# Optimization experiments

Hardware: AMD Instinct MI355X
Metric: run time of the kernel (lower is better)

The kernel has to match this reference:

```python
import jax, jax.numpy as jnp
import numpy as np

N_NODES = 50000
N_EDGES = 20000
NNZ = 500000


def _degrees(node_idx, edge_idx):
    ones = jnp.ones((node_idx.shape[0],), dtype=jnp.float32)
    deg_e = jax.ops.segment_sum(ones, edge_idx, num_segments=N_EDGES)
    deg_v = jax.ops.segment_sum(ones, node_idx, num_segments=N_NODES)
    return jnp.maximum(deg_e, 1.0)[:, None], jnp.maximum(deg_v, 1.0)[:, None]


def hgnn_conv(X, W, b, node_idx, edge_idx, deg_e, deg_v):
    # X: [V, Fin] -> project, V->E mean scatter, E->V mean gather (HGNN conv)
    H = X @ W                                                     # [V, Fout]
    e_feat = jax.ops.segment_sum(H[node_idx], edge_idx, num_segments=N_EDGES) / deg_e  # [E, Fout]
    v_feat = jax.ops.segment_sum(e_feat[edge_idx], node_idx, num_segments=N_NODES) / deg_v  # [V, Fout]
    return v_feat + b


def setup_inputs() -> dict:
    key = jax.random.key(0)
    ks = jax.random.split(key, 6)
    X = jax.random.normal(ks[0], (N_NODES, 256), dtype=jnp.float32)
    node_idx = jax.random.randint(ks[1], (NNZ,), 0, N_NODES, dtype=jnp.int32)
    edge_idx = jax.random.randint(ks[2], (NNZ,), 0, N_EDGES, dtype=jnp.int32)
    W1 = jax.random.normal(ks[3], (256, 256), dtype=jnp.float32) / np.sqrt(256.0)
    W2 = jax.random.normal(ks[4], (256, 256), dtype=jnp.float32) / np.sqrt(256.0)
    W3 = jax.random.normal(ks[5], (256, 40), dtype=jnp.float32) / np.sqrt(256.0)
    return {"X": X, "node_idx": node_idx, "edge_idx": edge_idx,
            "W1": W1, "b1": jnp.zeros((256,), jnp.float32),
            "W2": W2, "b2": jnp.zeros((256,), jnp.float32),
            "W3": W3, "b3": jnp.zeros((40,), jnp.float32)}


def reference(X, node_idx, edge_idx, W1, b1, W2, b2, W3, b3):
    deg_e, deg_v = _degrees(node_idx, edge_idx)
    # dropout layers are identity in eval mode
    H = jax.nn.relu(hgnn_conv(X, W1, b1, node_idx, edge_idx, deg_e, deg_v))
    H = jax.nn.relu(hgnn_conv(H, W2, b2, node_idx, edge_idx, deg_e, deg_v))
    H = hgnn_conv(H, W3, b3, node_idx, edge_idx, deg_e, deg_v)
    return jax.nn.log_softmax(H, axis=1)
```

## Files before the change

### kernel.cpp

```cpp
#include <hip/hip_runtime.h>
#include <math.h>

#define N_NODES 50000
#define N_EDGES 20000
#define NNZ_CT  500000
#define KDIM    256
#define K32     8

#define NB_RANK 62
#define CHUNK   8192
#define EW      5000
#define VW      12500

typedef __attribute__((ext_vector_type(8))) short    short8v;
typedef __attribute__((ext_vector_type(4))) float    f32x4;
typedef __attribute__((ext_vector_type(8))) unsigned short ushort8v;
typedef __attribute__((ext_vector_type(4))) unsigned short ushort4v;

#define GLD16(g, l) __builtin_amdgcn_global_load_lds( \
    (const __attribute__((address_space(1))) unsigned int*)(g), \
    (__attribute__((address_space(3))) unsigned int*)(l), 16, 0, 0)

__device__ __forceinline__ unsigned short bf16_rne(float f) {
    unsigned u = __float_as_uint(f);
    return (unsigned short)((u + 0x7FFFu + ((u >> 16) & 1u)) >> 16);
}
__device__ __forceinline__ float bf16_to_f(unsigned short h) {
    return __uint_as_float(((unsigned)h) << 16);
}
__device__ __forceinline__ void bf16_split(float f, unsigned short& h, unsigned short& l) {
    unsigned u = __float_as_uint(f);
    unsigned hb = (u + 0x7FFFu + ((u >> 16) & 1u)) >> 16;
    h = (unsigned short)hb;
    float r = f - __uint_as_float(hb << 16);
    unsigned ru = __float_as_uint(r);
    l = (unsigned short)((ru + 0x7FFFu + ((ru >> 16) & 1u)) >> 16);
}

__global__ __launch_bounds__(256) void rank_lds(
    const int* __restrict__ node_idx, const int* __restrict__ edge_idx,
    unsigned* __restrict__ bhe, unsigned* __restrict__ bhv,
    unsigned char* __restrict__ lrank_e, unsigned char* __restrict__ lrank_v)
{
    __shared__ unsigned hist[VW];
    int b = blockIdx.x;
    int i0 = b * CHUNK;
    int i1 = i0 + CHUNK; if (i1 > NNZ_CT) i1 = NNZ_CT;
    for (int w = threadIdx.x; w < EW; w += 256) hist[w] = 0;
    __syncthreads();
    for (int i = i0 + threadIdx.x; i < i1; i += 256) {
        int e = edge_idx[i];
        unsigned sh = 8u * (e & 3);
        unsigned old = atomicAdd(&hist[e >> 2], 1u << sh);
        lrank_e[i] = (unsigned char)((old >> sh) & 0xFFu);
    }
    __syncthreads();
    for (int w = threadIdx.x; w < EW; w += 256) bhe[b * EW + w] = hist[w];
    __syncthreads();
    for (int w = threadIdx.x; w < VW; w += 256) hist[w] = 0;
    __syncthreads();
    for (int i = i0 + threadIdx.x; i < i1; i += 256) {
        int v = node_idx[i];
        unsigned sh = 8u * (v & 3);
        unsigned old = atomicAdd(&hist[v >> 2], 1u << sh);
        lrank_v[i] = (unsigned char)((old >> sh) & 0xFFu);
    }
    __syncthreads();
    for (int w = threadIdx.x; w < VW; w += 256) bhv[b * VW + w] = hist[w];
}

__device__ __forceinline__ void conv_B_body(
    const float* __restrict__ B, unsigned short* __restrict__ Bh,
    unsigned short* __restrict__ Bl, int Ncols, int n16_count, int t)
{
    if (t >= n16_count * 512) return;
    int lane = t & 63, k32 = (t >> 6) & 7, n16 = t >> 9;
    int col = n16 * 16 + (lane & 15);
    int k0  = k32 * 32 + (lane >> 4) * 8;
    ushort8v h, l;
#pragma unroll
    for (int j = 0; j < 8; j++) {
        float f = (col < Ncols) ? B[(size_t)(k0 + j) * Ncols + col] : 0.f;
        unsigned short hh, ll; bf16_split(f, hh, ll); h[j] = hh; l[j] = ll;
    }
    size_t off = (((size_t)n16 * 8 + k32) << 9) + lane * 8;
    *(ushort8v*)(Bh + off) = h;
    *(ushort8v*)(Bl + off) = l;
}

__global__ __launch_bounds__(256) void mid_fuse(
    const unsigned* __restrict__ bhe, const unsigned* __restrict__ bhv,
    unsigned* __restrict__ bbase_e, unsigned* __restrict__ bbase_v,
    int* __restrict__ cnt_e, int* __restrict__ cnt_v,
    const float* __restrict__ X, unsigned short* __restrict__ Xb,
    const float* __restrict__ W1, unsigned short* __restrict__ W1h, unsigned short* __restrict__ W1l,
    const float* __restrict__ W2, unsigned short* __restrict__ W2h, unsigned short* __restrict__ W2l,
    const float* __restrict__ W3, unsigned short* __restrict__ W3h, unsigned short* __restrict__ W3l)
{
    int b0 = blockIdx.x;
    if (b0 < 69) {
        int t = b0 * 256 + threadIdx.x;
        if (t >= EW + VW) return;
        const unsigned* bh; unsigned* bb; int* cnt; int w;
        if (t < EW) { bh = bhe; bb = bbase_e; cnt = cnt_e; w = t; }
        else        { bh = bhv; bb = bbase_v; cnt = cnt_v; w = t - EW; }
        int stride = (t < EW) ? EW : VW;
        unsigned s0 = 0, s1 = 0, s2 = 0, s3 = 0;
#pragma unroll 2
        for (int b = 0; b < NB_RANK; ++b) {
            unsigned h = bh[(size_t)b * stride + w];
            bb[(size_t)b * stride + w] = s0 | (s1 << 8) | (s2 << 16) | (s3 << 24);
            s0 += h & 255u; s1 += (h >> 8) & 255u; s2 += (h >> 16) & 255u; s3 += (h >> 24);
        }
        *(int4*)(cnt + 4 * w) = make_int4((int)s0, (int)s1, (int)s2, (int)s3);
    } else if (b0 < 6319) {
        int t = (b0 - 69) * 256 + threadIdx.x;
        const float* src = X + (size_t)t * 8;
        float f[8];
        *(float4*)(f)     = *(const float4*)(src);
        *(float4*)(f + 4) = *(const float4*)(src + 4);
        ushort8v h;
#pragma unroll
        for (int j = 0; j < 8; j++) h[j] = bf16_rne(f[j]);
        *(ushort8v*)(Xb + (size_t)t * 8) = h;
    } else {
        int j = b0 - 6319;
        if (j < 32)      conv_B_body(W1, W1h, W1l, 256, 16, j * 256 + (int)threadIdx.x);
        else if (j < 64) conv_B_body(W2, W2h, W2l, 256, 16, (j - 32) * 256 + (int)threadIdx.x);
        else             conv_B_body(W3, W3h, W3l, 40,  8,  (j - 64) * 256 + (int)threadIdx.x);
    }
}

__global__ __launch_bounds__(1024) void scan_dual(
    const int* __restrict__ cnt_e, int* __restrict__ off_e, float* __restrict__ inv_e,
    const int* __restrict__ cnt_v, int* __restrict__ off_v, float* __restrict__ inv_v)
{
    const int* cnt; int* off; float* inv; int n;
    if (blockIdx.x == 0) { cnt = cnt_e; off = off_e; inv = inv_e; n = N_EDGES; }
    else                 { cnt = cnt_v; off = off_v; inv = inv_v; n = N_NODES; }
    __shared__ int wsum[16];
    __shared__ int carry_s;
    int tid = threadIdx.x, lane = tid & 63, wid = tid >> 6;
    if (tid == 0) carry_s = 0;
    __syncthreads();
    for (int base = 0; base < n; base += 4096) {
        int i4 = base + tid * 4;
        int4 x = make_int4(0, 0, 0, 0);
        if (i4 + 3 < n) x = *(const int4*)(cnt + i4);
        else if (i4 < n) {
            x.x = cnt[i4];
            if (i4 + 1 < n) x.y = cnt[i4 + 1];
            if (i4 + 2 < n) x.z = cnt[i4 + 2];
        }
        int s0 = x.x, s1 = s0 + x.y, s2 = s1 + x.z, s3 = s2 + x.w;
        int incl = s3;
#pragma unroll
        for (int o = 1; o < 64; o <<= 1) { int t = __shfl_up(incl, o, 64); if (lane >= o) incl += t; }
        if (lane == 63) wsum[wid] = incl;
        __syncthreads();
        if (wid == 0) {
            int v = (lane < 16) ? wsum[lane] : 0;
#pragma unroll
            for (int o = 1; o < 16; o <<= 1) { int t = __shfl_up(v, o, 64); if (lane >= o) v += t; }
            if (lane < 16) wsum[lane] = v;
        }
        __syncthreads();
        int wpre = (wid == 0) ? 0 : wsum[wid - 1];
        int carry = carry_s;
        int excl = carry + wpre + incl - s3;
        if (i4 < n) {
            int e0 = excl, e1 = excl + s0, e2 = excl + s1, e3 = excl + s2;
            if (i4 + 3 < n) { *(int4*)(off + i4) = make_int4(e0, e1, e2, e3); }
            else {
                off[i4] = e0;
                if (i4 + 1 < n) off[i4 + 1] = e1;
                if (i4 + 2 < n) off[i4 + 2] = e2;
            }
            inv[i4] = 1.0f / fmaxf((float)x.x, 1.0f);
            if (i4 + 1 < n) inv[i4 + 1] = 1.0f / fmaxf((float)x.y, 1.0f);
            if (i4 + 2 < n) inv[i4 + 2] = 1.0f / fmaxf((float)x.z, 1.0f);
            if (i4 + 3 < n) inv[i4 + 3] = 1.0f / fmaxf((float)x.w, 1.0f);
        }
        __syncthreads();
        if (tid == 1023) carry_s = carry + wpre + incl;
        __syncthreads();
    }
    if (tid == 0) off[n] = carry_s;
}

__global__ __launch_bounds__(256) void fill_part(
    const int* __restrict__ node_idx, const int* __restrict__ edge_idx,
    const unsigned char* __restrict__ lrank_e, const unsigned char* __restrict__ lrank_v,
    const unsigned* __restrict__ bbase_e, const unsigned* __restrict__ bbase_v,
    const int* __restrict__ off_e, const int* __restrict__ off_v,
    int* __restrict__ csr_e_nodes, int* __restrict__ csr_v_edges)
{
    int part = blockIdx.x & 7, blk = blockIdx.x >> 3, nblk = gridDim.x >> 3;
    int elo = part * (N_EDGES / 8), ehi = elo + N_EDGES / 8;
    int vlo = part * (N_NODES / 8), vhi = vlo + N_NODES / 8;
    for (int i = blk * 256 + threadIdx.x; i < NNZ_CT; i += nblk * 256) {
        int e = edge_idx[i], v = node_idx[i];
        int b = i >> 13;
        if (e >= elo && e < ehi) {
            unsigned bb = (bbase_e[(size_t)b * EW + (e >> 2)] >> (8u * (e & 3))) & 0xFFu;
            csr_e_nodes[off_e[e] + (int)bb + (int)lrank_e[i]] = v;
        }
        if (v >= vlo && v < vhi) {
            unsigned bb = (bbase_v[(size_t)b * VW + (v >> 2)] >> (8u * (v & 3))) & 0xFFu;
            csr_v_edges[off_v[v] + (int)bb + (int)lrank_v[i]] = e;
        }
    }
}

__global__ __launch_bounds__(256) void gemm_bf16(
    const unsigned short* __restrict__ At,
    const unsigned short* __restrict__ Bh, const unsigned short* __restrict__ Bl,
    unsigned short* __restrict__ C, int M, int Ncols, int ldC)
{
    __shared__ unsigned short lds[16384];
    const int tid  = threadIdx.x;
    const int lane = tid & 63, wid = tid >> 6;
    const int wr = wid >> 1, wc = wid & 1;
    const int m0t = blockIdx.y * 8;
    const int n0t = blockIdx.x * 8;

    f32x4 acc[4][4] = {};

    for (int k32 = 0; k32 < K32; ++k32) {
#pragma unroll
        for (int i = 0; i < 6; ++i) {
            int c = i * 4 + wid;
            if (c < 8) {
                const unsigned short* gA = At + (((size_t)(m0t + c) * 8 + k32) << 9) + lane * 8;
                GLD16(gA, &lds[c * 512 + lane * 8]);
            } else {
                int idx = c - 8, half = idx >> 3, st = idx & 7;
                const unsigned short* gB = (half ? Bl : Bh)
                    + (((size_t)(n0t + st) * 8 + k32) << 9) + lane * 8;
                GLD16(gB, &lds[4096 + idx * 512 + lane * 8]);
            }
        }
        __syncthreads();
        short8v a[4], bh[4], bl[4];
#pragma unroll
        for (int x = 0; x < 4; ++x) {
            a[x]  = *(const short8v*)&lds[(wr * 4 + x) * 512 + lane * 8];
            bh[x] = *(const short8v*)&lds[4096 + (wc * 4 + x) * 512 + lane * 8];
            bl[x] = *(const short8v*)&lds[4096 + (8 + wc * 4 + x) * 512 + lane * 8];
        }
#pragma unroll
        for (int mi = 0; mi < 4; ++mi)
#pragma unroll
            for (int ni = 0; ni < 4; ++ni) {
                acc[mi][ni] = __builtin_amdgcn_mfma_f32_16x16x32_bf16(a[mi], bh[ni], acc[mi][ni], 0, 0, 0);
                acc[mi][ni] = __builtin_amdgcn_mfma_f32_16x16x32_bf16(a[mi], bl[ni], acc[mi][ni], 0, 0, 0);
            }
        __syncthreads();
    }

    {
        const int rg = lane >> 4, cl = lane & 15;
        const int base = wid * 4096;
#pragma unroll
        for (int mi = 0; mi < 4; ++mi) {
            int swz = ((mi * 4 + rg) & 3) << 4;
#pragma unroll
            for (int ni = 0; ni < 4; ++ni) {
                int colf = (ni * 16 + cl) ^ swz;
#pragma unroll
                for (int r = 0; r < 4; ++r)
                    lds[base + (mi * 16 + rg * 4 + r) * 64 + colf] = bf16_rne(acc[mi][ni][r]);
            }
        }
    }
    __syncthreads();
    {
        int row = tid >> 1, half = tid & 1;
        int grow = blockIdx.y * 128 + row;
        if (grow < M) {
            int wsrc = (row >> 6) * 2 + half;
            int rl = row & 63;
            int swz = ((rl >> 2) & 3) << 4;
            unsigned short* dst = C + (size_t)grow * ldC + n0t * 16 + half * 64;
#pragma unroll
            for (int s = 0; s < 8; ++s) {
                int c0 = half * 64 + s * 8;
                if (n0t * 16 + c0 + 8 <= Ncols) {
                    ushort8v v = *(const ushort8v*)&lds[wsrc * 4096 + rl * 64 + ((s * 8) ^ swz)];
                    *(ushort8v*)(dst + s * 8) = v;
                }
            }
        }
    }
}

__global__ __launch_bounds__(256) void agg_e256_tiled(
    const unsigned short* __restrict__ src, unsigned short* __restrict__ Et,
    const int* __restrict__ offs, const int* __restrict__ lists,
    const float* __restrict__ invdeg)
{
    __shared__ unsigned short hbuf[16 * 264];
    int tid = threadIdx.x, lane = tid & 63, wid = tid >> 6;
    int e16 = blockIdx.x;
#pragma unroll
    for (int q = 0; q < 4; ++q) {
        int el = wid * 4 + q;
        int w = e16 * 16 + el;
        int s = offs[w], e = offs[w + 1];
        float a0 = 0.f, a1 = 0.f, a2 = 0.f, a3 = 0.f;
        for (int j = s; j < e; j += 8) {
            int r[8]; float m[8];
            r[0] = lists[j]; m[0] = 1.f;
#pragma unroll
            for (int u = 1; u < 8; ++u) {
                bool ok = (j + u) < e;
                r[u] = ok ? lists[j + u] : r[0];
                m[u] = ok ? 1.f : 0.f;
            }
            ushort4v v[8];
#pragma unroll
            for (int u = 0; u < 8; ++u)
                v[u] = *(const ushort4v*)(src + (size_t)r[u] * 256 + lane * 4);
            a0 += bf16_to_f(v[0][0]); a1 += bf16_to_f(v[0][1]);
            a2 += bf16_to_f(v[0][2]); a3 += bf16_to_f(v[0][3]);
#pragma unroll
            for (int u = 1; u < 8; ++u) {
                a0 = fmaf(m[u], bf16_to_f(v[u][0]), a0);
                a1 = fmaf(m[u], bf16_to_f(v[u][1]), a1);
                a2 = fmaf(m[u], bf16_to_f(v[u][2]), a2);
                a3 = fmaf(m[u], bf16_to_f(v[u][3]), a3);
            }
        }
        float sc = invdeg[w];
        ushort4v o;
        o[0] = bf16_rne(a0 * sc); o[1] = bf16_rne(a1 * sc);
        o[2] = bf16_rne(a2 * sc); o[3] = bf16_rne(a3 * sc);
        *(ushort4v*)&hbuf[el * 264 + lane * 4] = o;
    }
    __syncthreads();
#pragma unroll
    for (int u = 0; u < 2; ++u) {
        int sl = tid * 2 + u;
        int k32 = sl >> 6, lt = sl & 63;
        int row = lt & 15, hi = lt >> 4;
        int k0 = k32 * 32 + hi * 8;
        ushort8v v = *(const ushort8v*)&hbuf[row * 264 + k0];
        *(ushort8v*)(Et + (((size_t)e16 * 8 + k32) << 9) + lt * 8) = v;
    }
}

__global__ __launch_bounds__(256) void agg_v256_row(
    const unsigned short* __restrict__ src, unsigned short* __restrict__ Vb,
    const int* __restrict__ offs, const int* __restrict__ lists,
    const float* __restrict__ invdeg, const float* __restrict__ bias, int nseg)
{
    int w = (blockIdx.x * 256 + threadIdx.x) >> 6;
    int lane = threadIdx.x & 63;
    if (w >= nseg) return;
    int s = offs[w], e = offs[w + 1];
    float a0 = 0.f, a1 = 0.f, a2 = 0.f, a3 = 0.f;
    for (int j = s; j < e; j += 8) {
        int r[8]; float m[8];
        r[0] = lists[j]; m[0] = 1.f;
#pragma unroll
        for (int u = 1; u < 8; ++u) {
            bool ok = (j + u) < e;
            r[u] = ok ? lists[j + u] : r[0];
            m[u] = ok ? 1.f : 0.f;
        }
        ushort4v v[8];
#pragma unroll
        for (int u = 0; u < 8; ++u)
            v[u] = *(const ushort4v*)(src + (size_t)r[u] * 256 + lane * 4);
        a0 += bf16_to_f(v[0][0]); a1 += bf16_to_f(v[0][1]);
        a2 += bf16_to_f(v[0][2]); a3 += bf16_to_f(v[0][3]);
#pragma unroll
        for (int u = 1; u < 8; ++u) {
            a0 = fmaf(m[u], bf16_to_f(v[u][0]), a0);
            a1 = fmaf(m[u], bf16_to_f(v[u][1]), a1);
            a2 = fmaf(m[u], bf16_to_f(v[u][2]), a2);
            a3 = fmaf(m[u], bf16_to_f(v[u][3]), a3);
        }
    }
    float sc = invdeg[w];
    const float4 b = *(const float4*)(bias + lane * 4);
    ushort4v o;
    o[0] = bf16_rne(fmaxf(a0 * sc + b.x, 0.f));
    o[1] = bf16_rne(fmaxf(a1 * sc + b.y, 0.f));
    o[2] = bf16_rne(fmaxf(a2 * sc + b.z, 0.f));
    o[3] = bf16_rne(fmaxf(a3 * sc + b.w, 0.f));
    *(ushort4v*)(Vb + (size_t)w * 256 + lane * 4) = o;
}

__global__ __launch_bounds__(256) void agg_v256_blk(
    const unsigned short* __restrict__ src, unsigned short* __restrict__ At,
    const int* __restrict__ offs, const int* __restrict__ lists,
    const float* __restrict__ invdeg, const float* __restrict__ bias)
{
    __shared__ unsigned short hbuf[16 * 264];
    int tid = threadIdx.x, lane = tid & 63, wid = tid >> 6;
    int m16 = blockIdx.x;
    const float4 b = *(const float4*)(bias + lane * 4);
#pragma unroll
    for (int q = 0; q < 4; ++q) {
        int nl = wid * 4 + q;
        int w = m16 * 16 + nl;
        int s = offs[w], e = offs[w + 1];
        float a0 = 0.f, a1 = 0.f, a2 = 0.f, a3 = 0.f;
        for (int j = s; j < e; j += 8) {
            int r[8]; float m[8];
            r[0] = lists[j]; m[0] = 1.f;
#pragma unroll
            for (int u = 1; u < 8; ++u) {
                bool ok = (j + u) < e;
                r[u] = ok ? lists[j + u] : r[0];
                m[u] = ok ? 1.f : 0.f;
            }
            ushort4v v[8];
#pragma unroll
            for (int u = 0; u < 8; ++u)
                v[u] = *(const ushort4v*)(src + (size_t)r[u] * 256 + lane * 4);
            a0 += bf16_to_f(v[0][0]); a1 += bf16_to_f(v[0][1]);
            a2 += bf16_to_f(v[0][2]); a3 += bf16_to_f(v[0][3]);
#pragma unroll
            for (int u = 1; u < 8; ++u) {
                a0 = fmaf(m[u], bf16_to_f(v[u][0]), a0);
                a1 = fmaf(m[u], bf16_to_f(v[u][1]), a1);
                a2 = fmaf(m[u], bf16_to_f(v[u][2]), a2);
                a3 = fmaf(m[u], bf16_to_f(v[u][3]), a3);
            }
        }
        float sc = invdeg[w];
        ushort4v o;
        o[0] = bf16_rne(fmaxf(a0 * sc + b.x, 0.f));
        o[1] = bf16_rne(fmaxf(a1 * sc + b.y, 0.f));
        o[2] = bf16_rne(fmaxf(a2 * sc + b.z, 0.f));
        o[3] = bf16_rne(fmaxf(a3 * sc + b.w, 0.f));
        *(ushort4v*)&hbuf[nl * 264 + lane * 4] = o;
    }
    __syncthreads();
#pragma unroll
    for (int u = 0; u < 2; ++u) {
        int sl = tid * 2 + u;
        int k32 = sl >> 6, lt = sl & 63;
        int row = lt & 15, hi = lt >> 4;
        int k0 = k32 * 32 + hi * 8;
        ushort8v v = *(const ushort8v*)&hbuf[row * 264 + k0];
        *(ushort8v*)(At + (((size_t)m16 * 8 + k32) << 9) + lt * 8) = v;
    }
}

__global__ __launch_bounds__(256) void agg_mean40(
    const unsigned short* __restrict__ src, unsigned short* __restrict__ dst,
    const int* __restrict__ offs, const int* __restrict__ lists,
    const float* __restrict__ invdeg, int nseg)
{
    int w = (blockIdx.x * 256 + threadIdx.x) >> 6;
    int lane = threadIdx.x & 63;
    if (w >= nseg) return;
    int s = offs[w], e = offs[w + 1];
    if (lane < 40) {
        float acc = 0.f;
        for (int j = s; j < e; j += 8) {
            int r[8]; float m[8];
            r[0] = lists[j]; m[0] = 1.f;
#pragma unroll
            for (int u = 1; u < 8; ++u) {
                bool ok = (j + u) < e;
                r[u] = ok ? lists[j + u] : r[0];
                m[u] = ok ? 1.f : 0.f;
            }
            float v[8];
#pragma unroll
            for (int u = 0; u < 8; ++u)
                v[u] = bf16_to_f(src[(size_t)r[u] * 40 + lane]);
            acc += v[0];
#pragma unroll
            for (int u = 1; u < 8; ++u) acc = fmaf(m[u], v[u], acc);
        }
        dst[(size_t)w * 40 + lane] = bf16_rne(acc * invdeg[w]);
    }
}

__global__ __launch_bounds__(256) void agg_v40_lsm(
    const unsigned short* __restrict__ efeat, float* __restrict__ out,
    const int* __restrict__ offs, const int* __restrict__ lists,
    const float* __restrict__ invdeg, const float* __restrict__ bias,
    int nseg)
{
    int w = (blockIdx.x * 256 + threadIdx.x) >> 6;
    int lane = threadIdx.x & 63;
    if (w >= nseg) return;
    int s = offs[w], e = offs[w + 1];
    float acc = 0.f;
    if (lane < 40) {
        for (int j = s; j < e; j += 4) {
            int r[4]; float m[4];
            r[0] = lists[j]; m[0] = 1.f;
#pragma unroll
            for (int u = 1; u < 4; ++u) {
                bool ok = (j + u) < e;
                r[u] = ok ? lists[j + u] : r[0];
                m[u] = ok ? 1.f : 0.f;
            }
            float v[4];
#pragma unroll
            for (int u = 0; u < 4; ++u)
                v[u] = bf16_to_f(efeat[(size_t)r[u] * 40 + lane]);
            acc += v[0];
#pragma unroll
            for (int u = 1; u < 4; ++u) acc = fmaf(m[u], v[u], acc);
        }
    }
    float val = (lane < 40) ? (acc * invdeg[w] + bias[lane]) : -1e30f;
    float m = val;
#pragma unroll
    for (int o = 32; o; o >>= 1) m = fmaxf(m, __shfl_xor(m, o));
    float ex = (lane < 40) ? expf(val - m) : 0.f;
    float ssum = ex;
#pragma unroll
    for (int o = 32; o; o >>= 1) ssum += __shfl_xor(ssum, o);
    if (lane < 40) out[(size_t)w * 40 + lane] = val - m - logf(ssum);
}

extern "C" void kernel_launch(void* const* d_in, const int* in_sizes, int n_in,
                              void* d_out, int out_size, void* d_ws, size_t ws_size,
                              hipStream_t stream)
{
    const float* X        = (const float*)d_in[0];
    const int*   node_idx = (const int*)d_in[1];
    const int*   edge_idx = (const int*)d_in[2];
    const float* W1 = (const float*)d_in[3];
    const float* b1 = (const float*)d_in[4];
    const float* W2 = (const float*)d_in[5];
    const float* b2 = (const float*)d_in[6];
    const float* W3 = (const float*)d_in[7];
    const float* b3 = (const float*)d_in[8];
    float* out = (float*)d_out;

    char* p = (char*)d_ws;
    auto alloc = [&](size_t bytes) -> char* {
        char* r = p;
        p += (bytes + 255) & ~(size_t)255;
        return r;
    };
    int*   cnt_e = (int*)alloc((size_t)N_EDGES * 4);
    int*   cnt_v = (int*)alloc((size_t)N_NODES * 4);
    int*   off_e = (int*)alloc((size_t)(N_EDGES + 1) * 4);
    int*   off_v = (int*)alloc((size_t)(N_NODES + 1) * 4);
    float* inv_e = (float*)alloc((size_t)N_EDGES * 4);
    float* inv_v = (float*)alloc((size_t)N_NODES * 4);
    unsigned* bhe = (unsigned*)alloc((size_t)NB_RANK * EW * 4);
    unsigned* bhv = (unsigned*)alloc((size_t)NB_RANK * VW * 4);
    unsigned* bbase_e = (unsigned*)alloc((size_t)NB_RANK * EW * 4);
    unsigned* bbase_v = (unsigned*)alloc((size_t)NB_RANK * VW * 4);
    unsigned char* lrank_e = (unsigned char*)alloc((size_t)NNZ_CT);
    unsigned char* lrank_v = (unsigned char*)alloc((size_t)NNZ_CT);
    int*   csr_e = (int*)alloc((size_t)NNZ_CT * 4);
    int*   csr_v = (int*)alloc((size_t)NNZ_CT * 4);

    const int M16 = N_NODES / 16;
    const int M16_PAD = 391 * 8;
    const int E16 = N_EDGES / 16;
    const int E16_PAD = 157 * 8;
    unsigned short* Xb  = (unsigned short*)alloc((size_t)N_NODES * 256 * 2);
    unsigned short* At  = (unsigned short*)alloc((size_t)M16_PAD * 4096 * 2);
    unsigned short* Et  = (unsigned short*)alloc((size_t)E16_PAD * 4096 * 2);
    unsigned short* Ef  = (unsigned short*)alloc((size_t)N_EDGES * 256 * 2);
    unsigned short* W1h = (unsigned short*)alloc((size_t)16 * 4096 * 2);
    unsigned short* W1l = (unsigned short*)alloc((size_t)16 * 4096 * 2);
    unsigned short* W2h = (unsigned short*)alloc((size_t)16 * 4096 * 2);
    unsigned short* W2l = (unsigned short*)alloc((size_t)16 * 4096 * 2);
    unsigned short* W3h = (unsigned short*)alloc((size_t)8 * 4096 * 2);
    unsigned short* W3l = (unsigned short*)alloc((size_t)8 * 4096 * 2);
    unsigned short* C40 = (unsigned short*)alloc((size_t)N_NODES * 40 * 2);
    unsigned short* E40 = (unsigned short*)alloc((size_t)N_EDGES * 40 * 2);

    rank_lds<<<NB_RANK, 256, 0, stream>>>(node_idx, edge_idx, bhe, bhv, lrank_e, lrank_v);
    mid_fuse<<<6399, 256, 0, stream>>>(bhe, bhv, bbase_e, bbase_v, cnt_e, cnt_v,
                                       X, Xb, W1, W1h, W1l, W2, W2h, W2l, W3, W3h, W3l);
    scan_dual<<<2, 1024, 0, stream>>>(cnt_e, off_e, inv_e, cnt_v, off_v, inv_v);
    fill_part<<<2048, 256, 0, stream>>>(node_idx, edge_idx, lrank_e, lrank_v,
                                        bbase_e, bbase_v, off_e, off_v, csr_e, csr_v);

    dim3 gE_gemm(2, 157);
    dim3 gV_gemm(1, 391);
    const int gEw = (N_EDGES + 3) / 4;
    const int gVw = (N_NODES + 3) / 4;

    agg_e256_tiled<<<E16, 256, 0, stream>>>(Xb, Et, off_e, csr_e, inv_e);
    gemm_bf16<<<gE_gemm, 256, 0, stream>>>(Et, W1h, W1l, Ef, N_EDGES, 256, 256);
    agg_v256_row<<<gVw, 256, 0, stream>>>(Ef, Xb, off_v, csr_v, inv_v, b1, N_NODES);

    agg_e256_tiled<<<E16, 256, 0, stream>>>(Xb, Et, off_e, csr_e, inv_e);
    gemm_bf16<<<gE_gemm, 256, 0, stream>>>(Et, W2h, W2l, Ef, N_EDGES, 256, 256);
    agg_v256_blk<<<M16, 256, 0, stream>>>(Ef, At, off_v, csr_v, inv_v, b2);

    gemm_bf16<<<gV_gemm, 256, 0, stream>>>(At, W3h, W3l, C40, N_NODES, 40, 40);
    agg_mean40<<<gEw, 256, 0, stream>>>(C40, E40, off_e, csr_e, inv_e, N_EDGES);
    agg_v40_lsm<<<gVw, 256, 0, stream>>>(E40, out, off_v, csr_v, inv_v, b3, N_NODES);
    (void)in_sizes; (void)n_in; (void)out_size; (void)ws_size;
}
```

Before: 327.3 us.

## Sub-bucket CSR by neighbor index range for gather locality across blocks

The counting sort now keys each incidence by (segment, neighbor-range) rather than segment alone: edges get 4 node ranges and nodes get 2 edge ranges. The 16-row aggregation kernels then walk the neighbor ranges in the outer loop, so all rows of a block, and roughly all concurrent blocks, gather from the same slice of the source feature matrix at the same time. This is meant to improve L2 hit rate on the random gathers. In exchange it doubles the LDS histogram and the rank/scan arrays, lengthens the scan, and computes inverse degrees from offsets instead of a precomputed array.

```diff
diff --git a/kernel.cpp b/kernel.cpp
--- a/kernel.cpp
+++ b/kernel.cpp
@@ -9,8 +9,12 @@
 
 #define NB_RANK 62
 #define CHUNK   8192
-#define EW      5000
-#define VW      12500
+#define RE      4
+#define RV      2
+#define ERNG    12500
+#define VRNG    10000
+#define EW2     20000
+#define VW2     25000
 
 typedef __attribute__((ext_vector_type(8))) short    short8v;
 typedef __attribute__((ext_vector_type(4))) float    f32x4;
@@ -42,31 +46,33 @@
     unsigned* __restrict__ bhe, unsigned* __restrict__ bhv,
     unsigned char* __restrict__ lrank_e, unsigned char* __restrict__ lrank_v)
 {
-    __shared__ unsigned hist[VW];
+    __shared__ unsigned hist[VW2];
     int b = blockIdx.x;
     int i0 = b * CHUNK;
     int i1 = i0 + CHUNK; if (i1 > NNZ_CT) i1 = NNZ_CT;
-    for (int w = threadIdx.x; w < EW; w += 256) hist[w] = 0;
+    for (int w = threadIdx.x; w < EW2; w += 256) hist[w] = 0;
     __syncthreads();
     for (int i = i0 + threadIdx.x; i < i1; i += 256) {
-        int e = edge_idx[i];
-        unsigned sh = 8u * (e & 3);
-        unsigned old = atomicAdd(&hist[e >> 2], 1u << sh);
+        int e = edge_idx[i], v = node_idx[i];
+        int key = e * RE + v / ERNG;
+        unsigned sh = 8u * (key & 3);
+        unsigned old = atomicAdd(&hist[key >> 2], 1u << sh);
         lrank_e[i] = (unsigned char)((old >> sh) & 0xFFu);
     }
     __syncthreads();
-    for (int w = threadIdx.x; w < EW; w += 256) bhe[b * EW + w] = hist[w];
-    __syncthreads();
-    for (int w = threadIdx.x; w < VW; w += 256) hist[w] = 0;
+    for (int w = threadIdx.x; w < EW2; w += 256) bhe[(size_t)b * EW2 + w] = hist[w];
+    __syncthreads();
+    for (int w = threadIdx.x; w < VW2; w += 256) hist[w] = 0;
     __syncthreads();
     for (int i = i0 + threadIdx.x; i < i1; i += 256) {
-        int v = node_idx[i];
-        unsigned sh = 8u * (v & 3);
-        unsigned old = atomicAdd(&hist[v >> 2], 1u << sh);
+        int e = edge_idx[i], v = node_idx[i];
+        int key = v * RV + e / VRNG;
+        unsigned sh = 8u * (key & 3);
+        unsigned old = atomicAdd(&hist[key >> 2], 1u << sh);
         lrank_v[i] = (unsigned char)((old >> sh) & 0xFFu);
     }
     __syncthreads();
-    for (int w = threadIdx.x; w < VW; w += 256) bhv[b * VW + w] = hist[w];
+    for (int w = threadIdx.x; w < VW2; w += 256) bhv[(size_t)b * VW2 + w] = hist[w];
 }
 
 __device__ __forceinline__ void conv_B_body(
@@ -98,13 +104,12 @@
     const float* __restrict__ W3, unsigned short* __restrict__ W3h, unsigned short* __restrict__ W3l)
 {
     int b0 = blockIdx.x;
-    if (b0 < 69) {
+    if (b0 < 176) {
         int t = b0 * 256 + threadIdx.x;
-        if (t >= EW + VW) return;
-        const unsigned* bh; unsigned* bb; int* cnt; int w;
-        if (t < EW) { bh = bhe; bb = bbase_e; cnt = cnt_e; w = t; }
-        else        { bh = bhv; bb = bbase_v; cnt = cnt_v; w = t - EW; }
-        int stride = (t < EW) ? EW : VW;
+        if (t >= EW2 + VW2) return;
+        const unsigned* bh; unsigned* bb; int* cnt; int w; int stride;
+        if (t < EW2) { bh = bhe; bb = bbase_e; cnt = cnt_e; w = t; stride = EW2; }
+        else         { bh = bhv; bb = bbase_v; cnt = cnt_v; w = t - EW2; stride = VW2; }
         unsigned s0 = 0, s1 = 0, s2 = 0, s3 = 0;
 #pragma unroll 2
         for (int b = 0; b < NB_RANK; ++b) {
@@ -113,8 +118,8 @@
             s0 += h & 255u; s1 += (h >> 8) & 255u; s2 += (h >> 16) & 255u; s3 += (h >> 24);
         }
         *(int4*)(cnt + 4 * w) = make_int4((int)s0, (int)s1, (int)s2, (int)s3);
-    } else if (b0 < 6319) {
-        int t = (b0 - 69) * 256 + threadIdx.x;
+    } else if (b0 < 6426) {
+        int t = (b0 - 176) * 256 + threadIdx.x;
         const float* src = X + (size_t)t * 8;
         float f[8];
         *(float4*)(f)     = *(const float4*)(src);
@@ -124,7 +129,7 @@
         for (int j = 0; j < 8; j++) h[j] = bf16_rne(f[j]);
         *(ushort8v*)(Xb + (size_t)t * 8) = h;
     } else {
-        int j = b0 - 6319;
+        int j = b0 - 6426;
         if (j < 32)      conv_B_body(W1, W1h, W1l, 256, 16, j * 256 + (int)threadIdx.x);
         else if (j < 64) conv_B_body(W2, W2h, W2l, 256, 16, (j - 32) * 256 + (int)threadIdx.x);
         else             conv_B_body(W3, W3h, W3l, 40,  8,  (j - 64) * 256 + (int)threadIdx.x);
@@ -132,12 +137,12 @@
 }
 
 __global__ __launch_bounds__(1024) void scan_dual(
-    const int* __restrict__ cnt_e, int* __restrict__ off_e, float* __restrict__ inv_e,
-    const int* __restrict__ cnt_v, int* __restrict__ off_v, float* __restrict__ inv_v)
-{
-    const int* cnt; int* off; float* inv; int n;
-    if (blockIdx.x == 0) { cnt = cnt_e; off = off_e; inv = inv_e; n = N_EDGES; }
-    else                 { cnt = cnt_v; off = off_v; inv = inv_v; n = N_NODES; }
+    const int* __restrict__ cnt_e, int* __restrict__ off_e,
+    const int* __restrict__ cnt_v, int* __restrict__ off_v)
+{
+    const int* cnt; int* off; int n;
+    if (blockIdx.x == 0) { cnt = cnt_e; off = off_e; n = N_EDGES * RE; }
+    else                 { cnt = cnt_v; off = off_v; n = N_NODES * RV; }
     __shared__ int wsum[16];
     __shared__ int carry_s;
     int tid = threadIdx.x, lane = tid & 63, wid = tid >> 6;
@@ -176,10 +181,6 @@
                 if (i4 + 1 < n) off[i4 + 1] = e1;
                 if (i4 + 2 < n) off[i4 + 2] = e2;
             }
-            inv[i4] = 1.0f / fmaxf((float)x.x, 1.0f);
-            if (i4 + 1 < n) inv[i4 + 1] = 1.0f / fmaxf((float)x.y, 1.0f);
-            if (i4 + 2 < n) inv[i4 + 2] = 1.0f / fmaxf((float)x.z, 1.0f);
-            if (i4 + 3 < n) inv[i4 + 3] = 1.0f / fmaxf((float)x.w, 1.0f);
         }
         __syncthreads();
         if (tid == 1023) carry_s = carry + wpre + incl;
@@ -202,12 +203,14 @@
         int e = edge_idx[i], v = node_idx[i];
         int b = i >> 13;
         if (e >= elo && e < ehi) {
-            unsigned bb = (bbase_e[(size_t)b * EW + (e >> 2)] >> (8u * (e & 3))) & 0xFFu;
-            csr_e_nodes[off_e[e] + (int)bb + (int)lrank_e[i]] = v;
+            int key = e * RE + v / ERNG;
+            unsigned bb = (bbase_e[(size_t)b * EW2 + (key >> 2)] >> (8u * (key & 3))) & 0xFFu;
+            csr_e_nodes[off_e[key] + (int)bb + (int)lrank_e[i]] = v;
         }
         if (v >= vlo && v < vhi) {
-            unsigned bb = (bbase_v[(size_t)b * VW + (v >> 2)] >> (8u * (v & 3))) & 0xFFu;
-            csr_v_edges[off_v[v] + (int)bb + (int)lrank_v[i]] = e;
+            int key = v * RV + e / VRNG;
+            unsigned bb = (bbase_v[(size_t)b * VW2 + (key >> 2)] >> (8u * (key & 3))) & 0xFFu;
+            csr_v_edges[off_v[key] + (int)bb + (int)lrank_v[i]] = e;
         }
     }
 }
@@ -296,45 +299,51 @@
 
 __global__ __launch_bounds__(256) void agg_e256_tiled(
     const unsigned short* __restrict__ src, unsigned short* __restrict__ Et,
-    const int* __restrict__ offs, const int* __restrict__ lists,
-    const float* __restrict__ invdeg)
+    const int* __restrict__ offs, const int* __restrict__ lists)
 {
     __shared__ unsigned short hbuf[16 * 264];
     int tid = threadIdx.x, lane = tid & 63, wid = tid >> 6;
     int e16 = blockIdx.x;
+    float acc[4][4] = {};
+    for (int p = 0; p < RE; ++p) {
+#pragma unroll
+        for (int q = 0; q < 4; ++q) {
+            int w = e16 * 16 + wid * 4 + q;
+            int s = offs[w * RE + p], e = offs[w * RE + p + 1];
+            for (int j = s; j < e; j += 8) {
+                int r[8]; float m[8];
+                r[0] = lists[j]; m[0] = 1.f;
+#pragma unroll
+                for (int u = 1; u < 8; ++u) {
+                    bool ok = (j + u) < e;
+                    r[u] = ok ? lists[j + u] : r[0];
+                    m[u] = ok ? 1.f : 0.f;
+                }
+                ushort4v v[8];
+#pragma unroll
+                for (int u = 0; u < 8; ++u)
+                    v[u] = *(const ushort4v*)(src + (size_t)r[u] * 256 + lane * 4);
+                acc[q][0] += bf16_to_f(v[0][0]); acc[q][1] += bf16_to_f(v[0][1]);
+                acc[q][2] += bf16_to_f(v[0][2]); acc[q][3] += bf16_to_f(v[0][3]);
+#pragma unroll
+                for (int u = 1; u < 8; ++u) {
+                    acc[q][0] = fmaf(m[u], bf16_to_f(v[u][0]), acc[q][0]);
+                    acc[q][1] = fmaf(m[u], bf16_to_f(v[u][1]), acc[q][1]);
+                    acc[q][2] = fmaf(m[u], bf16_to_f(v[u][2]), acc[q][2]);
+                    acc[q][3] = fmaf(m[u], bf16_to_f(v[u][3]), acc[q][3]);
+                }
+            }
+        }
+    }
 #pragma unroll
     for (int q = 0; q < 4; ++q) {
         int el = wid * 4 + q;
         int w = e16 * 16 + el;
-        int s = offs[w], e = offs[w + 1];
-        float a0 = 0.f, a1 = 0.f, a2 = 0.f, a3 = 0.f;
-        for (int j = s; j < e; j += 8) {
-            int r[8]; float m[8];
-            r[0] = lists[j]; m[0] = 1.f;
-#pragma unroll
-            for (int u = 1; u < 8; ++u) {
-                bool ok = (j + u) < e;
-                r[u] = ok ? lists[j + u] : r[0];
-                m[u] = ok ? 1.f : 0.f;
-            }
-            ushort4v v[8];
-#pragma unroll
-            for (int u = 0; u < 8; ++u)
-                v[u] = *(const ushort4v*)(src + (size_t)r[u] * 256 + lane * 4);
-            a0 += bf16_to_f(v[0][0]); a1 += bf16_to_f(v[0][1]);
-            a2 += bf16_to_f(v[0][2]); a3 += bf16_to_f(v[0][3]);
-#pragma unroll
-            for (int u = 1; u < 8; ++u) {
-                a0 = fmaf(m[u], bf16_to_f(v[u][0]), a0);
-                a1 = fmaf(m[u], bf16_to_f(v[u][1]), a1);
-                a2 = fmaf(m[u], bf16_to_f(v[u][2]), a2);
-                a3 = fmaf(m[u], bf16_to_f(v[u][3]), a3);
-            }
-        }
-        float sc = invdeg[w];
+        int deg = offs[(w + 1) * RE] - offs[w * RE];
+        float sc = 1.0f / (float)((deg > 1) ? deg : 1);
         ushort4v o;
-        o[0] = bf16_rne(a0 * sc); o[1] = bf16_rne(a1 * sc);
-        o[2] = bf16_rne(a2 * sc); o[3] = bf16_rne(a3 * sc);
+        o[0] = bf16_rne(acc[q][0] * sc); o[1] = bf16_rne(acc[q][1] * sc);
+        o[2] = bf16_rne(acc[q][2] * sc); o[3] = bf16_rne(acc[q][3] * sc);
         *(ushort4v*)&hbuf[el * 264 + lane * 4] = o;
     }
     __syncthreads();
@@ -352,37 +361,40 @@
 __global__ __launch_bounds__(256) void agg_v256_row(
     const unsigned short* __restrict__ src, unsigned short* __restrict__ Vb,
     const int* __restrict__ offs, const int* __restrict__ lists,
-    const float* __restrict__ invdeg, const float* __restrict__ bias, int nseg)
+    const float* __restrict__ bias, int nseg)
 {
     int w = (blockIdx.x * 256 + threadIdx.x) >> 6;
     int lane = threadIdx.x & 63;
     if (w >= nseg) return;
-    int s = offs[w], e = offs[w + 1];
     float a0 = 0.f, a1 = 0.f, a2 = 0.f, a3 = 0.f;
-    for (int j = s; j < e; j += 8) {
-        int r[8]; float m[8];
-        r[0] = lists[j]; m[0] = 1.f;
-#pragma unroll
-        for (int u = 1; u < 8; ++u) {
-            bool ok = (j + u) < e;
-            r[u] = ok ? lists[j + u] : r[0];
-            m[u] = ok ? 1.f : 0.f;
-        }
-        ushort4v v[8];
-#pragma unroll
-        for (int u = 0; u < 8; ++u)
-            v[u] = *(const ushort4v*)(src + (size_t)r[u] * 256 + lane * 4);
-        a0 += bf16_to_f(v[0][0]); a1 += bf16_to_f(v[0][1]);
-        a2 += bf16_to_f(v[0][2]); a3 += bf16_to_f(v[0][3]);
-#pragma unroll
-        for (int u = 1; u < 8; ++u) {
-            a0 = fmaf(m[u], bf16_to_f(v[u][0]), a0);
-            a1 = fmaf(m[u], bf16_to_f(v[u][1]), a1);
-            a2 = fmaf(m[u], bf16_to_f(v[u][2]), a2);
-            a3 = fmaf(m[u], bf16_to_f(v[u][3]), a3);
-        }
-    }
-    float sc = invdeg[w];
+    for (int p = 0; p < RV; ++p) {
+        int s = offs[w * RV + p], e = offs[w * RV + p + 1];
+        for (int j = s; j < e; j += 8) {
+            int r[8]; float m[8];
+            r[0] = lists[j]; m[0] = 1.f;
+#pragma unroll
+            for (int u = 1; u < 8; ++u) {
+                bool ok = (j + u) < e;
+                r[u] = ok ? lists[j + u] : r[0];
+                m[u] = ok ? 1.f : 0.f;
+            }
+            ushort4v v[8];
+#pragma unroll
+            for (int u = 0; u < 8; ++u)
+                v[u] = *(const ushort4v*)(src + (size_t)r[u] * 256 + lane * 4);
+            a0 += bf16_to_f(v[0][0]); a1 += bf16_to_f(v[0][1]);
+            a2 += bf16_to_f(v[0][2]); a3 += bf16_to_f(v[0][3]);
+#pragma unroll
+            for (int u = 1; u < 8; ++u) {
+                a0 = fmaf(m[u], bf16_to_f(v[u][0]), a0);
+                a1 = fmaf(m[u], bf16_to_f(v[u][1]), a1);
+                a2 = fmaf(m[u], bf16_to_f(v[u][2]), a2);
+                a3 = fmaf(m[u], bf16_to_f(v[u][3]), a3);
+            }
+        }
+    }
+    int deg = offs[(w + 1) * RV] - offs[w * RV];
+    float sc = 1.0f / (float)((deg > 1) ? deg : 1);
     const float4 b = *(const float4*)(bias + lane * 4);
     ushort4v o;
     o[0] = bf16_rne(fmaxf(a0 * sc + b.x, 0.f));
@@ -395,47 +407,54 @@
 __global__ __launch_bounds__(256) void agg_v256_blk(
     const unsigned short* __restrict__ src, unsigned short* __restrict__ At,
     const int* __restrict__ offs, const int* __restrict__ lists,
-    const float* __restrict__ invdeg, const float* __restrict__ bias)
+    const float* __restrict__ bias)
 {
     __shared__ unsigned short hbuf[16 * 264];
     int tid = threadIdx.x, lane = tid & 63, wid = tid >> 6;
     int m16 = blockIdx.x;
     const float4 b = *(const float4*)(bias + lane * 4);
+    float acc[4][4] = {};
+    for (int p = 0; p < RV; ++p) {
+#pragma unroll
+        for (int q = 0; q < 4; ++q) {
+            int w = m16 * 16 + wid * 4 + q;
+            int s = offs[w * RV + p], e = offs[w * RV + p + 1];
+            for (int j = s; j < e; j += 8) {
+                int r[8]; float m[8];
+                r[0] = lists[j]; m[0] = 1.f;
+#pragma unroll
+                for (int u = 1; u < 8; ++u) {
+                    bool ok = (j + u) < e;
+                    r[u] = ok ? lists[j + u] : r[0];
+                    m[u] = ok ? 1.f : 0.f;
+                }
+                ushort4v v[8];
+#pragma unroll
+                for (int u = 0; u < 8; ++u)
+                    v[u] = *(const ushort4v*)(src + (size_t)r[u] * 256 + lane * 4);
+                acc[q][0] += bf16_to_f(v[0][0]); acc[q][1] += bf16_to_f(v[0][1]);
+                acc[q][2] += bf16_to_f(v[0][2]); acc[q][3] += bf16_to_f(v[0][3]);
+#pragma unroll
+                for (int u = 1; u < 8; ++u) {
+                    acc[q][0] = fmaf(m[u], bf16_to_f(v[u][0]), acc[q][0]);
+                    acc[q][1] = fmaf(m[u], bf16_to_f(v[u][1]), acc[q][1]);
+                    acc[q][2] = fmaf(m[u], bf16_to_f(v[u][2]), acc[q][2]);
+                    acc[q][3] = fmaf(m[u], bf16_to_f(v[u][3]), acc[q][3]);
+                }
+            }
+        }
+    }
 #pragma unroll
     for (int q = 0; q < 4; ++q) {
         int nl = wid * 4 + q;
         int w = m16 * 16 + nl;
-        int s = offs[w], e = offs[w + 1];
-        float a0 = 0.f, a1 = 0.f, a2 = 0.f, a3 = 0.f;
-        for (int j = s; j < e; j += 8) {
-            int r[8]; float m[8];
-            r[0] = lists[j]; m[0] = 1.f;
-#pragma unroll
-            for (int u = 1; u < 8; ++u) {
-                bool ok = (j + u) < e;
-                r[u] = ok ? lists[j + u] : r[0];
-                m[u] = ok ? 1.f : 0.f;
-            }
-            ushort4v v[8];
-#pragma unroll
-            for (int u = 0; u < 8; ++u)
-                v[u] = *(const ushort4v*)(src + (size_t)r[u] * 256 + lane * 4);
-            a0 += bf16_to_f(v[0][0]); a1 += bf16_to_f(v[0][1]);
-            a2 += bf16_to_f(v[0][2]); a3 += bf16_to_f(v[0][3]);
-#pragma unroll
-            for (int u = 1; u < 8; ++u) {
-                a0 = fmaf(m[u], bf16_to_f(v[u][0]), a0);
-                a1 = fmaf(m[u], bf16_to_f(v[u][1]), a1);
-                a2 = fmaf(m[u], bf16_to_f(v[u][2]), a2);
-                a3 = fmaf(m[u], bf16_to_f(v[u][3]), a3);
-            }
-        }
-        float sc = invdeg[w];
+        int deg = offs[(w + 1) * RV] - offs[w * RV];
+        float sc = 1.0f / (float)((deg > 1) ? deg : 1);
         ushort4v o;
-        o[0] = bf16_rne(fmaxf(a0 * sc + b.x, 0.f));
-        o[1] = bf16_rne(fmaxf(a1 * sc + b.y, 0.f));
-        o[2] = bf16_rne(fmaxf(a2 * sc + b.z, 0.f));
-        o[3] = bf16_rne(fmaxf(a3 * sc + b.w, 0.f));
+        o[0] = bf16_rne(fmaxf(acc[q][0] * sc + b.x, 0.f));
+        o[1] = bf16_rne(fmaxf(acc[q][1] * sc + b.y, 0.f));
+        o[2] = bf16_rne(fmaxf(acc[q][2] * sc + b.z, 0.f));
+        o[3] = bf16_rne(fmaxf(acc[q][3] * sc + b.w, 0.f));
         *(ushort4v*)&hbuf[nl * 264 + lane * 4] = o;
     }
     __syncthreads();
@@ -453,12 +472,13 @@
 __global__ __launch_bounds__(256) void agg_mean40(
     const unsigned short* __restrict__ src, unsigned short* __restrict__ dst,
     const int* __restrict__ offs, const int* __restrict__ lists,
-    const float* __restrict__ invdeg, int nseg)
+    int nseg)
 {
     int w = (blockIdx.x * 256 + threadIdx.x) >> 6;
     int lane = threadIdx.x & 63;
     if (w >= nseg) return;
-    int s = offs[w], e = offs[w + 1];
+    int s = offs[w * RE], e = offs[(w + 1) * RE];
+    int deg = e - s;
     if (lane < 40) {
         float acc = 0.f;
         for (int j = s; j < e; j += 8) {
@@ -478,20 +498,21 @@
 #pragma unroll
             for (int u = 1; u < 8; ++u) acc = fmaf(m[u], v[u], acc);
         }
-        dst[(size_t)w * 40 + lane] = bf16_rne(acc * invdeg[w]);
+        float sc = 1.0f / (float)((deg > 1) ? deg : 1);
+        dst[(size_t)w * 40 + lane] = bf16_rne(acc * sc);
     }
 }
 
 __global__ __launch_bounds__(256) void agg_v40_lsm(
     const unsigned short* __restrict__ efeat, float* __restrict__ out,
     const int* __restrict__ offs, const int* __restrict__ lists,
-    const float* __restrict__ invdeg, const float* __restrict__ bias,
-    int nseg)
+    const float* __restrict__ bias, int nseg)
 {
     int w = (blockIdx.x * 256 + threadIdx.x) >> 6;
     int lane = threadIdx.x & 63;
     if (w >= nseg) return;
-    int s = offs[w], e = offs[w + 1];
+    int s = offs[w * RV], e = offs[(w + 1) * RV];
+    int deg = e - s;
     float acc = 0.f;
     if (lane < 40) {
         for (int j = s; j < e; j += 4) {
@@ -512,7 +533,8 @@
             for (int u = 1; u < 4; ++u) acc = fmaf(m[u], v[u], acc);
         }
     }
-    float val = (lane < 40) ? (acc * invdeg[w] + bias[lane]) : -1e30f;
+    float sc = 1.0f / (float)((deg > 1) ? deg : 1);
+    float val = (lane < 40) ? (acc * sc + bias[lane]) : -1e30f;
     float m = val;
 #pragma unroll
     for (int o = 32; o; o >>= 1) m = fmaxf(m, __shfl_xor(m, o));
@@ -544,16 +566,14 @@
         p += (bytes + 255) & ~(size_t)255;
         return r;
     };
-    int*   cnt_e = (int*)alloc((size_t)N_EDGES * 4);
-    int*   cnt_v = (int*)alloc((size_t)N_NODES * 4);
-    int*   off_e = (int*)alloc((size_t)(N_EDGES + 1) * 4);
-    int*   off_v = (int*)alloc((size_t)(N_NODES + 1) * 4);
-    float* inv_e = (float*)alloc((size_t)N_EDGES * 4);
-    float* inv_v = (float*)alloc((size_t)N_NODES * 4);
-    unsigned* bhe = (unsigned*)alloc((size_t)NB_RANK * EW * 4);
-    unsigned* bhv = (unsigned*)alloc((size_t)NB_RANK * VW * 4);
-    unsigned* bbase_e = (unsigned*)alloc((size_t)NB_RANK * EW * 4);
-    unsigned* bbase_v = (unsigned*)alloc((size_t)NB_RANK * VW * 4);
+    int*   cnt_e = (int*)alloc((size_t)N_EDGES * RE * 4);
+    int*   cnt_v = (int*)alloc((size_t)N_NODES * RV * 4);
+    int*   off_e = (int*)alloc((size_t)(N_EDGES * RE + 1) * 4);
+    int*   off_v = (int*)alloc((size_t)(N_NODES * RV + 1) * 4);
+    unsigned* bhe = (unsigned*)alloc((size_t)NB_RANK * EW2 * 4);
+    unsigned* bhv = (unsigned*)alloc((size_t)NB_RANK * VW2 * 4);
+    unsigned* bbase_e = (unsigned*)alloc((size_t)NB_RANK * EW2 * 4);
+    unsigned* bbase_v = (unsigned*)alloc((size_t)NB_RANK * VW2 * 4);
     unsigned char* lrank_e = (unsigned char*)alloc((size_t)NNZ_CT);
     unsigned char* lrank_v = (unsigned char*)alloc((size_t)NNZ_CT);
     int*   csr_e = (int*)alloc((size_t)NNZ_CT * 4);
@@ -577,9 +597,9 @@
     unsigned short* E40 = (unsigned short*)alloc((size_t)N_EDGES * 40 * 2);
 
     rank_lds<<<NB_RANK, 256, 0, stream>>>(node_idx, edge_idx, bhe, bhv, lrank_e, lrank_v);
-    mid_fuse<<<6399, 256, 0, stream>>>(bhe, bhv, bbase_e, bbase_v, cnt_e, cnt_v,
+    mid_fuse<<<6506, 256, 0, stream>>>(bhe, bhv, bbase_e, bbase_v, cnt_e, cnt_v,
                                        X, Xb, W1, W1h, W1l, W2, W2h, W2l, W3, W3h, W3l);
-    scan_dual<<<2, 1024, 0, stream>>>(cnt_e, off_e, inv_e, cnt_v, off_v, inv_v);
+    scan_dual<<<2, 1024, 0, stream>>>(cnt_e, off_e, cnt_v, off_v);
     fill_part<<<2048, 256, 0, stream>>>(node_idx, edge_idx, lrank_e, lrank_v,
                                         bbase_e, bbase_v, off_e, off_v, csr_e, csr_v);
 
@@ -588,16 +608,16 @@
     const int gEw = (N_EDGES + 3) / 4;
     const int gVw = (N_NODES + 3) / 4;
 
-    agg_e256_tiled<<<E16, 256, 0, stream>>>(Xb, Et, off_e, csr_e, inv_e);
+    agg_e256_tiled<<<E16, 256, 0, stream>>>(Xb, Et, off_e, csr_e);
     gemm_bf16<<<gE_gemm, 256, 0, stream>>>(Et, W1h, W1l, Ef, N_EDGES, 256, 256);
-    agg_v256_row<<<gVw, 256, 0, stream>>>(Ef, Xb, off_v, csr_v, inv_v, b1, N_NODES);
-
-    agg_e256_tiled<<<E16, 256, 0, stream>>>(Xb, Et, off_e, csr_e, inv_e);
+    agg_v256_row<<<gVw, 256, 0, stream>>>(Ef, Xb, off_v, csr_v, b1, N_NODES);
+
+    agg_e256_tiled<<<E16, 256, 0, stream>>>(Xb, Et, off_e, csr_e);
     gemm_bf16<<<gE_gemm, 256, 0, stream>>>(Et, W2h, W2l, Ef, N_EDGES, 256, 256);
-    agg_v256_blk<<<M16, 256, 0, stream>>>(Ef, At, off_v, csr_v, inv_v, b2);
+    agg_v256_blk<<<M16, 256, 0, stream>>>(Ef, At, off_v, csr_v, b2);
 
     gemm_bf16<<<gV_gemm, 256, 0, stream>>>(At, W3h, W3l, C40, N_NODES, 40, 40);
-    agg_mean40<<<gEw, 256, 0, stream>>>(C40, E40, off_e, csr_e, inv_e, N_EDGES);
-    agg_v40_lsm<<<gVw, 256, 0, stream>>>(E40, out, off_v, csr_v, inv_v, b3, N_NODES);
+    agg_mean40<<<gEw, 256, 0, stream>>>(C40, E40, off_e, csr_e, N_EDGES);
+    agg_v40_lsm<<<gVw, 256, 0, stream>>>(E40, out, off_v, csr_v, b3, N_NODES);
     (void)in_sizes; (void)n_in; (void)out_size; (void)ws_size;
 }
```

Result: slower. 360.3 us (+10.1%).
